# Kernel tuning notes

Hardware: AMD Instinct MI355X
Metric: run time of the kernel (lower is better)

The kernel has to match this reference:

```python
import jax, jax.numpy as jnp
import numpy as np

EPS = 1e-5

def mean_variance_norm(feat):
    # feat: [B, C, H, W]; torch .var(dim=2) is unbiased (ddof=1)
    b, c, h, w = feat.shape
    flat = feat.reshape(b, c, h * w)
    mean = flat.mean(axis=2)[:, :, None, None]
    var = flat.var(axis=2, ddof=1) + EPS
    std = jnp.sqrt(var)[:, :, None, None]
    return (feat - mean) / std

def conv1x1(x, W, b):
    # 1x1 conv == per-pixel linear: [B,Cin,H,W] x [Cout,Cin] -> [B,Cout,H,W]
    return jnp.einsum('oc,bchw->bohw', W, x) + b[None, :, None, None]

def setup_inputs() -> dict:
    key = jax.random.key(0)
    ks = jax.random.split(key, 8)
    B, C, H, W = 4, 256, 64, 64
    scale = 1.0 / np.sqrt(C)
    return {
        'content': jax.random.normal(ks[0], (B, C, H, W), jnp.float32),
        'style':   jax.random.normal(ks[1], (B, C, H, W), jnp.float32),
        'Wf': jax.random.normal(ks[2], (C, C), jnp.float32) * scale,
        'bf': jnp.zeros((C,), jnp.float32),
        'Wg': jax.random.normal(ks[3], (C, C), jnp.float32) * scale,
        'bg': jnp.zeros((C,), jnp.float32),
        'Wh': jax.random.normal(ks[4], (C, C), jnp.float32) * scale,
        'bh': jnp.zeros((C,), jnp.float32),
    }

def reference(content, style, Wf, bf, Wg, bg, Wh, bh):
    b, c, h, w = content.shape
    hw = h * w
    # keys are detached in the original
    content_key = mean_variance_norm(jax.lax.stop_gradient(content))
    style_key = mean_variance_norm(jax.lax.stop_gradient(style))
    Fq = conv1x1(content_key, Wf, bf).reshape(b, -1, hw).transpose(0, 2, 1)  # [b, hw, ck]
    G = conv1x1(style_key, Wg, bg).reshape(b, -1, hw)                       # [b, ck, hw]
    Hv = conv1x1(style, Wh, bh).reshape(b, -1, hw).transpose(0, 2, 1)       # [b, hw, c]
    S = jax.nn.softmax(jnp.einsum('bik,bkj->bij', Fq, G), axis=-1)          # [b, hw, hw]
    mean = jnp.einsum('bij,bjc->bic', S, Hv)                                # [b, hw, c]
    second = jnp.einsum('bij,bjc->bic', S, Hv * Hv)
    std = jnp.sqrt(jax.nn.relu(second - mean * mean))
    mean = mean.reshape(b, h, w, c).transpose(0, 3, 1, 2)                   # [b, c, h, w]
    std = std.reshape(b, h, w, c).transpose(0, 3, 1, 2)
    out = std * mean_variance_norm(content) + mean
    return (out, mean, std)
```

## Files before the change

kernel.cpp:

```cpp
#include <hip/hip_runtime.h>
#include <hip/hip_fp16.h>
#include <math.h>

#define HW 4096
#define NC 256
#define NB 4
#define EPSF 1e-5f
#define TEN (NB * HW * NC)

typedef _Float16 half8 __attribute__((ext_vector_type(8)));
typedef _Float16 half4v __attribute__((ext_vector_type(4)));
typedef float f32x4 __attribute__((ext_vector_type(4)));
typedef unsigned int u32;

#define STATS_BYTES (4096 * 4)
#define QF_OFF  (STATS_BYTES)
#define KF_OFF  (QF_OFF + TEN * 2)
#define VF_OFF  (KF_OFF + TEN * 2)

typedef const __attribute__((address_space(1))) void* gas_vp;
typedef __attribute__((address_space(3))) void* las_vp;
__device__ __forceinline__ void gload_lds16(const void* g, void* l) {
  __builtin_amdgcn_global_load_lds((gas_vp)g, (las_vp)l, 16, 0, 0);
}

__global__ __launch_bounds__(256) void stats_kernel(
    const float* __restrict__ content, const float* __restrict__ style,
    float* __restrict__ ws) {
  int bc = blockIdx.x;
  int t = threadIdx.x;
  const float* src = (bc < 1024 ? content : style) + (size_t)(bc & 1023) * HW;
  const float4* s4 = (const float4*)src;
  float sum = 0.f, ss = 0.f;
#pragma unroll
  for (int n = 0; n < 4; ++n) {
    float4 v = s4[t + n * 256];
    sum += v.x + v.y + v.z + v.w;
    ss += v.x * v.x + v.y * v.y + v.z * v.z + v.w * v.w;
  }
#pragma unroll
  for (int m = 1; m < 64; m <<= 1) {
    sum += __shfl_xor(sum, m, 64);
    ss += __shfl_xor(ss, m, 64);
  }
  __shared__ float redS[4], redQ[4];
  int w = t >> 6;
  if ((t & 63) == 0) { redS[w] = sum; redQ[w] = ss; }
  __syncthreads();
  if (t == 0) {
    float S = redS[0] + redS[1] + redS[2] + redS[3];
    float Q2 = redQ[0] + redQ[1] + redQ[2] + redQ[3];
    float mean = S * (1.0f / HW);
    float var = (Q2 - S * mean) * (1.0f / (HW - 1));
    float rstd = rsqrtf(var + EPSF);
    float* meanArr = ws + (bc < 1024 ? 0 : 2048);
    float* rstdArr = meanArr + 1024;
    meanArr[bc & 1023] = mean;
    rstdArr[bc & 1023] = rstd;
  }
}

__global__ __launch_bounds__(256) void proj_kernel(
    const float* __restrict__ content, const float* __restrict__ style,
    const float* __restrict__ Wf, const float* __restrict__ bf,
    const float* __restrict__ Wg, const float* __restrict__ bg,
    const float* __restrict__ Wh, const float* __restrict__ bh,
    char* __restrict__ wsb) {
  float* ws = (float*)wsb;
  int pt = blockIdx.x;
  int ot = blockIdx.y;
  int z = blockIdx.z;
  int tensor = z >> 2, b = z & 3;

  const float* X; const float* Wm; const float* bias;
  const float* meanA = nullptr; const float* rstdA = nullptr;
  if (tensor == 0)      { X = content; Wm = Wf; bias = bf; meanA = ws;        rstdA = ws + 1024; }
  else if (tensor == 1) { X = style;   Wm = Wg; bias = bg; meanA = ws + 2048; rstdA = ws + 3072; }
  else                  { X = style;   Wm = Wh; bias = bh; }

  __shared__ float Xs[32 * 132];
  __shared__ float Wt[32 * 68];

  int t = threadIdx.x;
  int p0 = pt * 128, o0 = ot * 64;
  int o_base = (t >> 4) * 4;
  int p_base = (t & 15) * 8;

  float bb[4];
  { float4 b4 = *(const float4*)&bias[o0 + o_base];
    bb[0] = b4.x; bb[1] = b4.y; bb[2] = b4.z; bb[3] = b4.w; }
  float acc[4][8];
#pragma unroll
  for (int oo = 0; oo < 4; ++oo)
#pragma unroll
    for (int pp = 0; pp < 8; ++pp) acc[oo][pp] = bb[oo];

  const float4* X4 = (const float4*)X;
  const float4* Wm4 = (const float4*)Wm;

  for (int kc = 0; kc < 8; ++kc) {
    int k0 = kc * 32;
    __syncthreads();
#pragma unroll
    for (int n = 0; n < 4; ++n) {
      int f = t + n * 256;
      int kk = f >> 5, p4 = f & 31;
      float4 v = X4[(size_t)(b * NC + k0 + kk) * (HW / 4) + (p0 / 4) + p4];
      if (tensor < 2) {
        float mC = meanA[b * NC + k0 + kk], rC = rstdA[b * NC + k0 + kk];
        v.x = (v.x - mC) * rC; v.y = (v.y - mC) * rC;
        v.z = (v.z - mC) * rC; v.w = (v.w - mC) * rC;
      }
      *(float4*)&Xs[kk * 132 + p4 * 4] = v;
    }
#pragma unroll
    for (int n = 0; n < 2; ++n) {
      int f = t + n * 256;
      int o = f >> 3, k4 = f & 7;
      float4 v = Wm4[(size_t)(o0 + o) * (NC / 4) + kc * 8 + k4];
      Wt[(k4 * 4 + 0) * 68 + o] = v.x;
      Wt[(k4 * 4 + 1) * 68 + o] = v.y;
      Wt[(k4 * 4 + 2) * 68 + o] = v.z;
      Wt[(k4 * 4 + 3) * 68 + o] = v.w;
    }
    __syncthreads();
#pragma unroll
    for (int kk = 0; kk < 32; ++kk) {
      float4 w4 = *(float4*)&Wt[kk * 68 + o_base];
      float4 xa = *(float4*)&Xs[kk * 132 + p_base];
      float4 xb = *(float4*)&Xs[kk * 132 + p_base + 4];
      float wv[4] = {w4.x, w4.y, w4.z, w4.w};
      float xv[8] = {xa.x, xa.y, xa.z, xa.w, xb.x, xb.y, xb.z, xb.w};
#pragma unroll
      for (int oo = 0; oo < 4; ++oo)
#pragma unroll
        for (int pp = 0; pp < 8; ++pp)
          acc[oo][pp] = fmaf(wv[oo], xv[pp], acc[oo][pp]);
    }
  }

  if (tensor < 2) {
    _Float16* dst = (_Float16*)(wsb + (tensor == 0 ? QF_OFF : KF_OFF));
#pragma unroll
    for (int pp = 0; pp < 8; ++pp) {
      half4v h;
      h[0] = (_Float16)acc[0][pp]; h[1] = (_Float16)acc[1][pp];
      h[2] = (_Float16)acc[2][pp]; h[3] = (_Float16)acc[3][pp];
      *(half4v*)&dst[((size_t)(b * HW) + p0 + p_base + pp) * 256 + o0 + o_base] = h;
    }
  } else {
    _Float16* dV = (_Float16*)(wsb + VF_OFF);
#pragma unroll
    for (int oo = 0; oo < 4; ++oo) {
      int ch = o0 + o_base + oo;
      half8 hv;
#pragma unroll
      for (int pp = 0; pp < 8; ++pp) hv[pp] = (_Float16)acc[oo][pp];
      size_t base = ((size_t)(b * NC) + ch) * HW + p0 + p_base;
      *(half8*)&dV[base] = hv;
    }
  }
}

__global__ __launch_bounds__(256, 3) void attn_kernel(
    char* __restrict__ wsb, const float* __restrict__ content,
    float* __restrict__ dout) {
  const _Float16* Qf = (const _Float16*)(wsb + QF_OFF);
  const _Float16* Kf = (const _Float16*)(wsb + KF_OFF);
  const _Float16* Vf = (const _Float16*)(wsb + VF_OFF);
  const float* meanC = (const float*)wsb;
  const float* rstdC = meanC + 1024;

  int raw = blockIdx.x;
  int xcd = raw & 7;
  int b = xcd >> 1;
  int qt = ((raw >> 3) << 1) | (xcd & 1);
  int q0 = qt * 32;

  int t = threadIdx.x;
  int lane = t & 63;
  int w = t >> 6;
  int qh = w >> 1;
  int chh = w & 1;
  int ml = lane & 15;
  int kg4 = lane >> 4;
  int lo = kg4 & 1, hi = kg4 >> 1;

  __shared__ int4 smem[2048];
  _Float16* Kt0h = (_Float16*)smem;
  _Float16* Kt1h = (_Float16*)(smem + 1024);

  half8 Qb[8];
#pragma unroll
  for (int ks = 0; ks < 8; ++ks) {
    size_t off = ((size_t)(b * HW) + q0 + qh * 16 + ml) * 256 + ks * 32 + kg4 * 8;
    Qb[ks] = *(const half8*)(Qf + off);
  }

  f32x4 accm[8], accs[8];
#pragma unroll
  for (int nt = 0; nt < 8; ++nt) {
    accm[nt] = (f32x4){0.f, 0.f, 0.f, 0.f};
    accs[nt] = (f32x4){0.f, 0.f, 0.f, 0.f};
  }
  float mrun = -INFINITY;
  float lrun = 0.f;

  const int4* Kg = (const int4*)(Kf + (size_t)b * HW * 256);
  const int4* Vg = (const int4*)(Vf + (size_t)b * NC * HW);
  int vrow = chh * 128 + ml;

  int ksrc[4];
  {
    int l5 = lane >> 5;
    int l31 = lane & 31;
#pragma unroll
    for (int j = 0; j < 4; ++j) {
      int c = (w * 4 + j) * 2 + l5;
      ksrc[j] = (l31 ^ c) * 32 + c;
    }
  }

#pragma unroll
  for (int j = 0; j < 4; ++j)
    gload_lds16(Kg + (size_t)ksrc[j], smem + (w * 4 + j) * 64);
  asm volatile("s_waitcnt vmcnt(0)" ::: "memory");
  __builtin_amdgcn_s_barrier();

#define TILE_BODY(KT, RB, SB)                                                  \
  {                                                                            \
    int kt_ = (KT);                                                            \
    int ktn_ = (kt_ + 1) & 127;                                                \
    _Pragma("unroll")                                                          \
    for (int j = 0; j < 4; ++j)                                                \
      gload_lds16(Kg + (size_t)ktn_ * 1024 + ksrc[j], (SB) + (w * 4 + j) * 64);\
    int4 vr0[4];                                                               \
    _Pragma("unroll")                                                          \
    for (int n = 0; n < 4; ++n)                                                \
      vr0[n] = Vg[(size_t)(vrow + n * 16) * (HW / 8) + kt_ * 4 + kg4];         \
    f32x4 S0 = (f32x4){0.f, 0.f, 0.f, 0.f};                                    \
    f32x4 S1 = (f32x4){0.f, 0.f, 0.f, 0.f};                                    \
    _Pragma("unroll")                                                          \
    for (int ks = 0; ks < 8; ++ks) {                                           \
      int c = ks * 4 + kg4;                                                    \
      half8 Ka0 = *(const half8*)((RB) + (c * 32 + (ml ^ c)) * 8);             \
      half8 Ka1 = *(const half8*)((RB) + (c * 32 + ((16 + ml) ^ c)) * 8);      \
      S0 = __builtin_amdgcn_mfma_f32_16x16x32_f16(Ka0, Qb[ks], S0, 0, 0, 0);   \
      S1 = __builtin_amdgcn_mfma_f32_16x16x32_f16(Ka1, Qb[ks], S1, 0, 0, 0);   \
    }                                                                          \
                     \
    float tm = fmaxf(fmaxf(fmaxf(S0[0], S0[1]), fmaxf(S0[2], S0[3])),          \
                     fmaxf(fmaxf(S1[0], S1[1]), fmaxf(S1[2], S1[3])));         \
    if (__any((int)(tm > mrun + 8.0f))) {                                      \
      float tr = fmaxf(tm, __shfl_xor(tm, 16, 64));                            \
      tr = fmaxf(tr, __shfl_xor(tr, 32, 64));                                  \
      float mn = fmaxf(mrun, tr);                                              \
      float a = __expf(mrun - mn);                                             \
      mrun = mn;                                                               \
      lrun *= a;                                                               \
       \
       \
      float a4[4];                                                             \
      _Pragma("unroll")                                                        \
      for (int r = 0; r < 4; ++r) a4[r] = __shfl(a, kg4 * 4 + r, 16);          \
      _Pragma("unroll")                                                        \
      for (int nt = 0; nt < 8; ++nt)                                           \
        _Pragma("unroll")                                                      \
        for (int r = 0; r < 4; ++r) { accm[nt][r] *= a4[r]; accs[nt][r] *= a4[r]; } \
    }                                                                          \
    _Float16 phv[8];                                                           \
    float rs = 0.f;                                                            \
    _Pragma("unroll")                                                          \
    for (int r = 0; r < 4; ++r) {                                              \
      _Float16 h0 = (_Float16)__expf(S0[r] - mrun);                            \
      _Float16 h1 = (_Float16)__expf(S1[r] - mrun);                            \
      phv[r] = h0; phv[4 + r] = h1;                                            \
      rs += (float)h0 + (float)h1;                                             \
    }                                                                          \
    lrun += rs;                                                                \
    half8 Pa;                                                                  \
    {                                                                          \
      union Hp { _Float16 h[2]; u32 u; };                                      \
      Hp pA0, pA1, pB0, pB1;                                                   \
      pA0.h[0] = phv[0]; pA0.h[1] = phv[1];                                    \
      pA1.h[0] = phv[2]; pA1.h[1] = phv[3];                                    \
      pB0.h[0] = phv[4]; pB0.h[1] = phv[5];                                    \
      pB1.h[0] = phv[6]; pB1.h[1] = phv[7];                                    \
      u32 A0 = pA0.u, A1 = pA1.u, B0 = pB0.u, B1 = pB1.u;                      \
      u32 oA0 = __shfl_xor((int)A0, 16, 64);                                   \
      u32 oA1 = __shfl_xor((int)A1, 16, 64);                                   \
      u32 oB0 = __shfl_xor((int)B0, 16, 64);                                   \
      u32 oB1 = __shfl_xor((int)B1, 16, 64);                                   \
      u32 n0[4], n1[4];                                                        \
      n0[0] = lo ? oA0 : A0; n0[1] = lo ? oA1 : A1;                            \
      n0[2] = lo ? A0 : oA0; n0[3] = lo ? A1 : oA1;                            \
      n1[0] = lo ? oB0 : B0; n1[1] = lo ? oB1 : B1;                            \
      n1[2] = lo ? B0 : oB0; n1[3] = lo ? B1 : oB1;                            \
      union Pu { u32 u[4]; half8 v; } fin;                                     \
      _Pragma("unroll")                                                        \
      for (int i = 0; i < 4; ++i) {                                            \
        u32 s = hi ? n0[i] : n1[i];                                            \
        u32 r2 = __shfl_xor((int)s, 32, 64);                                   \
        fin.u[i] = (hi == lo) ? (hi ? n1[i] : n0[i]) : r2;                     \
      }                                                                        \
      Pa = fin.v;                                                              \
    }                                                                          \
    int4 vr1[4];                                                               \
    _Pragma("unroll")                                                          \
    for (int n = 0; n < 4; ++n)                                                \
      vr1[n] = Vg[(size_t)(vrow + (n + 4) * 16) * (HW / 8) + kt_ * 4 + kg4];   \
    _Pragma("unroll")                                                          \
    for (int n = 0; n < 8; ++n) {                                              \
      union { int4 i; half8 v; __half2 h2[4]; } bv;                            \
      bv.i = (n < 4) ? vr0[n] : vr1[n - 4];                                    \
      union { half8 v; __half2 h2[4]; } bh, bl;                                \
      _Pragma("unroll")                                                        \
      for (int u = 0; u < 4; ++u) {                                            \
        __half2 hh = __hmul2(bv.h2[u], bv.h2[u]);                              \
        bh.h2[u] = hh;                                                         \
        bl.h2[u] = __hfma2(bv.h2[u], bv.h2[u], __hneg2(hh));                   \
      }                                                                        \
      accm[n] = __builtin_amdgcn_mfma_f32_16x16x32_f16(Pa, bv.v, accm[n], 0, 0, 0); \
      accs[n] = __builtin_amdgcn_mfma_f32_16x16x32_f16(Pa, bh.v, accs[n], 0, 0, 0); \
      accs[n] = __builtin_amdgcn_mfma_f32_16x16x32_f16(Pa, bl.v, accs[n], 0, 0, 0); \
    }                                                                          \
    asm volatile("s_waitcnt vmcnt(0)" ::: "memory");                           \
    __builtin_amdgcn_s_barrier();                                              \
  }

  for (int kt2 = 0; kt2 < 64; ++kt2) {
    TILE_BODY(2 * kt2, Kt0h, smem + 1024);
    TILE_BODY(2 * kt2 + 1, Kt1h, smem);
  }
#undef TILE_BODY

  {
    lrun += __shfl_xor(lrun, 16, 64);
    lrun += __shfl_xor(lrun, 32, 64);
  }
  float invl = 1.0f / lrun;
  float invl4[4];
#pragma unroll
  for (int r = 0; r < 4; ++r)
    invl4[r] = __shfl(invl, kg4 * 4 + r, 16);

#pragma unroll
  for (int nt = 0; nt < 8; ++nt)
#pragma unroll
    for (int r = 0; r < 4; ++r) {
      float mu = accm[nt][r] * invl4[r];
      float s2 = accs[nt][r] * invl4[r];
      accm[nt][r] = mu;
      accs[nt][r] = sqrtf(fmaxf(s2 - mu * mu, 0.f));
    }

  __syncthreads();
  float* MUL = (float*)smem;
  float* SDL = MUL + 32 * 36;
#pragma unroll 1
  for (int ph2 = 0; ph2 < 8; ++ph2) {
    __syncthreads();
    if (chh == (ph2 >> 2)) {
      int ntb = (ph2 & 3) * 2;
#pragma unroll
      for (int nn = 0; nn < 2; ++nn)
#pragma unroll
        for (int r = 0; r < 4; ++r) {
          int row32 = nn * 16 + ml;
          int ql = qh * 16 + kg4 * 4 + r;
          MUL[row32 * 36 + ql] = accm[ntb + nn][r];
          SDL[row32 * 36 + ql] = accs[ntb + nn][r];
        }
    }
    __syncthreads();
    int qq = (t & 7) * 4;
    int chl = t >> 3;
    int ch = ph2 * 32 + chl;
    float4 mu4 = *(float4*)&MUL[chl * 36 + qq];
    float4 sd4 = *(float4*)&SDL[chl * 36 + qq];
    size_t base = ((size_t)(b * NC) + ch) * HW + q0 + qq;
    float4 c4 = *(const float4*)&content[base];
    float mC = meanC[b * NC + ch];
    float rC = rstdC[b * NC + ch];
    float4 o4;
    o4.x = sd4.x * ((c4.x - mC) * rC) + mu4.x;
    o4.y = sd4.y * ((c4.y - mC) * rC) + mu4.y;
    o4.z = sd4.z * ((c4.z - mC) * rC) + mu4.z;
    o4.w = sd4.w * ((c4.w - mC) * rC) + mu4.w;
    *(float4*)&dout[base] = o4;
    *(float4*)&dout[TEN + base] = mu4;
    *(float4*)&dout[2 * TEN + base] = sd4;
  }
}

extern "C" void kernel_launch(void* const* d_in, const int* in_sizes, int n_in,
                              void* d_out, int out_size, void* d_ws, size_t ws_size,
                              hipStream_t stream) {
  const float* content = (const float*)d_in[0];
  const float* style   = (const float*)d_in[1];
  const float* Wf = (const float*)d_in[2];
  const float* bf = (const float*)d_in[3];
  const float* Wg = (const float*)d_in[4];
  const float* bg = (const float*)d_in[5];
  const float* Wh = (const float*)d_in[6];
  const float* bh = (const float*)d_in[7];
  char* wsb = (char*)d_ws;
  float* out = (float*)d_out;

  hipLaunchKernelGGL(stats_kernel, dim3(2048), dim3(256), 0, stream,
                     content, style, (float*)wsb);
  hipLaunchKernelGGL(proj_kernel, dim3(32, 4, 12), dim3(256), 0, stream,
                     content, style, Wf, bf, Wg, bg, Wh, bh, wsb);
  hipLaunchKernelGGL(attn_kernel, dim3(512), dim3(256), 0, stream,
                     wsb, content, out);
}
```

Baseline: 751.3 us.

## Software-pipeline QK scores one tile ahead of softmax and PV accumulation

Restructures the flash-attention inner loop so the QK^T MFMAs for the next key tile are computed while the softmax and PV MFMAs of the current tile proceed. The K tile prefetch now runs two tiles ahead, and the barrier moves to the top of each iteration. The second half of the V loads is also issued earlier. This aims to overlap score computation with the value accumulation, at the cost of extra live registers for the pending score tile and a reordered barrier scheme that has to stay correct across the double buffer.

```diff
diff --git a/kernel.cpp b/kernel.cpp
--- a/kernel.cpp
+++ b/kernel.cpp
@@ -226,29 +226,49 @@
     gload_lds16(Kg + (size_t)ksrc[j], smem + (w * 4 + j) * 64);
   asm volatile("s_waitcnt vmcnt(0)" ::: "memory");
   __builtin_amdgcn_s_barrier();
-
-#define TILE_BODY(KT, RB, SB)                                                  \
+#pragma unroll
+  for (int j = 0; j < 4; ++j)
+    gload_lds16(Kg + (size_t)(1024 + ksrc[j]), smem + 1024 + (w * 4 + j) * 64);
+
+  f32x4 S0 = (f32x4){0.f, 0.f, 0.f, 0.f};
+  f32x4 S1 = (f32x4){0.f, 0.f, 0.f, 0.f};
+#pragma unroll
+  for (int ks = 0; ks < 8; ++ks) {
+    int c = ks * 4 + kg4;
+    half8 Ka0 = *(const half8*)(Kt0h + (c * 32 + (ml ^ c)) * 8);
+    half8 Ka1 = *(const half8*)(Kt0h + (c * 32 + ((16 + ml) ^ c)) * 8);
+    S0 = __builtin_amdgcn_mfma_f32_16x16x32_f16(Ka0, Qb[ks], S0, 0, 0, 0);
+    S1 = __builtin_amdgcn_mfma_f32_16x16x32_f16(Ka1, Qb[ks], S1, 0, 0, 0);
+  }
+
+#define ITER_BODY(KT, QB, GT)                                                  \
   {                                                                            \
     int kt_ = (KT);                                                            \
-    int ktn_ = (kt_ + 1) & 127;                                                \
+    asm volatile("s_waitcnt vmcnt(0)" ::: "memory");                           \
+    __builtin_amdgcn_s_barrier();                                              \
+    int ktn_ = (kt_ + 2) & 127;                                                \
     _Pragma("unroll")                                                          \
     for (int j = 0; j < 4; ++j)                                                \
-      gload_lds16(Kg + (size_t)ktn_ * 1024 + ksrc[j], (SB) + (w * 4 + j) * 64);\
+      gload_lds16(Kg + (size_t)ktn_ * 1024 + ksrc[j], (GT) + (w * 4 + j) * 64);\
     int4 vr0[4];                                                               \
     _Pragma("unroll")                                                          \
     for (int n = 0; n < 4; ++n)                                                \
       vr0[n] = Vg[(size_t)(vrow + n * 16) * (HW / 8) + kt_ * 4 + kg4];         \
-    f32x4 S0 = (f32x4){0.f, 0.f, 0.f, 0.f};                                    \
-    f32x4 S1 = (f32x4){0.f, 0.f, 0.f, 0.f};                                    \
+    f32x4 T0 = (f32x4){0.f, 0.f, 0.f, 0.f};                                    \
+    f32x4 T1 = (f32x4){0.f, 0.f, 0.f, 0.f};                                    \
     _Pragma("unroll")                                                          \
     for (int ks = 0; ks < 8; ++ks) {                                           \
       int c = ks * 4 + kg4;                                                    \
-      half8 Ka0 = *(const half8*)((RB) + (c * 32 + (ml ^ c)) * 8);             \
-      half8 Ka1 = *(const half8*)((RB) + (c * 32 + ((16 + ml) ^ c)) * 8);      \
-      S0 = __builtin_amdgcn_mfma_f32_16x16x32_f16(Ka0, Qb[ks], S0, 0, 0, 0);   \
-      S1 = __builtin_amdgcn_mfma_f32_16x16x32_f16(Ka1, Qb[ks], S1, 0, 0, 0);   \
+      half8 Ka0 = *(const half8*)((QB) + (c * 32 + (ml ^ c)) * 8);             \
+      half8 Ka1 = *(const half8*)((QB) + (c * 32 + ((16 + ml) ^ c)) * 8);      \
+      T0 = __builtin_amdgcn_mfma_f32_16x16x32_f16(Ka0, Qb[ks], T0, 0, 0, 0);   \
+      T1 = __builtin_amdgcn_mfma_f32_16x16x32_f16(Ka1, Qb[ks], T1, 0, 0, 0);   \
     }                                                                          \
-                     \
+    int4 vr1[4];                                                               \
+    _Pragma("unroll")                                                          \
+    for (int n = 0; n < 4; ++n)                                                \
+      vr1[n] = Vg[(size_t)(vrow + (n + 4) * 16) * (HW / 8) + kt_ * 4 + kg4];   \
+                           \
     float tm = fmaxf(fmaxf(fmaxf(S0[0], S0[1]), fmaxf(S0[2], S0[3])),          \
                      fmaxf(fmaxf(S1[0], S1[1]), fmaxf(S1[2], S1[3])));         \
     if (__any((int)(tm > mrun + 8.0f))) {                                      \
@@ -258,8 +278,6 @@
       float a = __expf(mrun - mn);                                             \
       mrun = mn;                                                               \
       lrun *= a;                                                               \
-       \
-       \
       float a4[4];                                                             \
       _Pragma("unroll")                                                        \
       for (int r = 0; r < 4; ++r) a4[r] = __shfl(a, kg4 * 4 + r, 16);          \
@@ -305,10 +323,6 @@
       }                                                                        \
       Pa = fin.v;                                                              \
     }                                                                          \
-    int4 vr1[4];                                                               \
-    _Pragma("unroll")                                                          \
-    for (int n = 0; n < 4; ++n)                                                \
-      vr1[n] = Vg[(size_t)(vrow + (n + 4) * 16) * (HW / 8) + kt_ * 4 + kg4];   \
     _Pragma("unroll")                                                          \
     for (int n = 0; n < 8; ++n) {                                              \
       union { int4 i; half8 v; __half2 h2[4]; } bv;                            \
@@ -324,15 +338,15 @@
       accs[n] = __builtin_amdgcn_mfma_f32_16x16x32_f16(Pa, bh.v, accs[n], 0, 0, 0); \
       accs[n] = __builtin_amdgcn_mfma_f32_16x16x32_f16(Pa, bl.v, accs[n], 0, 0, 0); \
     }                                                                          \
-    asm volatile("s_waitcnt vmcnt(0)" ::: "memory");                           \
-    __builtin_amdgcn_s_barrier();                                              \
+    S0 = T0;                                                                   \
+    S1 = T1;                                                                   \
   }
 
   for (int kt2 = 0; kt2 < 64; ++kt2) {
-    TILE_BODY(2 * kt2, Kt0h, smem + 1024);
-    TILE_BODY(2 * kt2 + 1, Kt1h, smem);
-  }
-#undef TILE_BODY
+    ITER_BODY(2 * kt2, Kt1h, smem);
+    ITER_BODY(2 * kt2 + 1, Kt0h, smem + 1024);
+  }
+#undef ITER_BODY
 
   {
     lrun += __shfl_xor(lrun, 16, 64);
```

After: 1.628 ms. 2.17x slower.
